# Performance work log

Hardware: AMD Instinct MI355X
Metric: run time of the kernel (lower is better)

## Reference

```python
import jax, jax.numpy as jnp
import numpy as np

D_EMB = 256
SCALE = 0.02
B, T = 4, 4096
EPS = 1e-5


def layer_norm(x, w, b):
    m = jnp.mean(x, axis=-1, keepdims=True)
    v = jnp.mean((x - m) ** 2, axis=-1, keepdims=True)
    return (x - m) * jax.lax.rsqrt(v + EPS) * w + b


def setup_inputs() -> dict:
    key = jax.random.key(0)
    ks = jax.random.split(key, 4)
    x = jax.random.normal(ks[0], (B, T, D_EMB), dtype=jnp.float32)
    qkv = jax.random.normal(ks[1], (3, D_EMB, D_EMB), dtype=jnp.float32) * SCALE
    # nn.Linear(D, 2D, bias=False): weight shape (2D, D), applied as x @ W.T
    w1 = jax.random.normal(ks[2], (2 * D_EMB, D_EMB), dtype=jnp.float32) * (1.0 / np.sqrt(D_EMB))
    w2 = jax.random.normal(ks[3], (D_EMB, 2 * D_EMB), dtype=jnp.float32) * (1.0 / np.sqrt(2 * D_EMB))
    ones = jnp.ones((D_EMB,), dtype=jnp.float32)
    zeros = jnp.zeros((D_EMB,), dtype=jnp.float32)
    return {
        "x": x, "qkv": qkv,
        "ln_q_w": ones, "ln_q_b": zeros,
        "ln_k_w": ones, "ln_k_b": zeros,
        "ln_attn_w": ones, "ln_attn_b": zeros,
        "w1": w1, "w2": w2,
        "ln_ff_w": ones, "ln_ff_b": zeros,
    }


def reference(x, qkv, ln_q_w, ln_q_b, ln_k_w, ln_k_b, ln_attn_w, ln_attn_b, w1, w2, ln_ff_w, ln_ff_b):
    # QKV projections: [3, B, T, D]
    y = jnp.einsum('btd,ndD->nbtD', x, qkv)
    q, k, v = y[0], y[1], y[2]
    q = layer_norm(q, ln_q_w, ln_q_b)
    k = layer_norm(k, ln_k_w, ln_k_b)
    # full (non-causal) single-head attention, scale by sqrt(D_EMB)
    scores = jnp.einsum('btd,bsd->bts', q, k) / jnp.sqrt(jnp.float32(D_EMB))
    attn = jax.nn.softmax(scores, axis=-1)
    y = jnp.einsum('bts,bsd->btd', attn, v)
    y = layer_norm(y, ln_attn_w, ln_attn_b)
    x = 0.7 * (x + y)
    # FFN with dual leaky_relu
    y = jax.nn.leaky_relu(x @ w1.T, negative_slope=0.2)
    y = jax.nn.leaky_relu(y @ w2.T, negative_slope=0.2)
    y = layer_norm(y, ln_ff_w, ln_ff_b)
    return 0.7 * (x + y)
```

## Files before the change

kernel.cpp:

```cpp
#include <hip/hip_runtime.h>

#define BSZ   4
#define TSEQ  4096
#define DEMB  256
#define NTOK  (BSZ * TSEQ)
#define HID   512
#define SPLITS 4
#define KEYS_PER_SPLIT (TSEQ / SPLITS)
#define TK 32
#define NT (KEYS_PER_SPLIT / TK)
#define KIMG_STRIDE 8704
#define VIMG_STRIDE 10240

using bf16x8 = __attribute__((ext_vector_type(8))) short;
using f32x16 = __attribute__((ext_vector_type(16))) float;

static __device__ __forceinline__ unsigned short f2bf(float f) {
  union { float f; unsigned u; } v; v.f = f;
  unsigned r = v.u + 0x7FFF + ((v.u >> 16) & 1);
  return (unsigned short)(r >> 16);
}
static __device__ __forceinline__ float bf2f(unsigned short u) {
  union { unsigned u; float f; } v; v.u = ((unsigned)u) << 16;
  return v.f;
}

static __device__ __forceinline__ void async16(void* lds, const void* gp) {
  __builtin_amdgcn_global_load_lds(
      (const __attribute__((address_space(1))) unsigned int*)gp,
      (__attribute__((address_space(3))) unsigned int*)lds, 16, 0, 0);
}

__global__ __launch_bounds__(256) void prep_kernel(
    const float* __restrict__ qkv, const float* __restrict__ w1,
    const float* __restrict__ w2, unsigned short* __restrict__ qkvT,
    unsigned short* __restrict__ w1b, unsigned short* __restrict__ w2b)
{
  const int tid = threadIdx.x;
  if (blockIdx.y < 3) {
    if (blockIdx.x >= 16) return;
    __shared__ float Ts[64][65];
    const int z  = blockIdx.y;
    const int k0 = (blockIdx.x >> 2) * 64;
    const int j0 = (blockIdx.x & 3) * 64;
    const float* src = qkv + (size_t)z * DEMB * DEMB + (size_t)k0 * DEMB + j0;
#pragma unroll
    for (int p = 0; p < 4; ++p) {
      int idx = p * 256 + tid;
      int r = idx >> 4, g = idx & 15;
      float4 v = *(const float4*)(src + (size_t)r * DEMB + g * 4);
      Ts[r][g * 4 + 0] = v.x; Ts[r][g * 4 + 1] = v.y;
      Ts[r][g * 4 + 2] = v.z; Ts[r][g * 4 + 3] = v.w;
    }
    __syncthreads();
    unsigned short* dst = qkvT + (size_t)z * DEMB * DEMB + (size_t)j0 * DEMB + k0;
#pragma unroll
    for (int p = 0; p < 4; ++p) {
      int idx = p * 256 + tid;
      int r = idx >> 4, g = idx & 15;
      ushort4 o;
      o.x = f2bf(Ts[g * 4 + 0][r]); o.y = f2bf(Ts[g * 4 + 1][r]);
      o.z = f2bf(Ts[g * 4 + 2][r]); o.w = f2bf(Ts[g * 4 + 3][r]);
      *(ushort4*)(dst + (size_t)r * DEMB + g * 4) = o;
    }
  } else {
    const float* s = (blockIdx.y == 3) ? w1 : w2;
    unsigned short* d = (blockIdx.y == 3) ? w1b : w2b;
    const int i = blockIdx.x * 256 + tid;
    float4 v = ((const float4*)s)[i];
    ushort4 o;
    o.x = f2bf(v.x); o.y = f2bf(v.y); o.z = f2bf(v.z); o.w = f2bf(v.w);
    ((ushort4*)d)[i] = o;
  }
}

__global__ __launch_bounds__(512, 1) void qkvln_kernel(
    const float* __restrict__ x, const unsigned short* __restrict__ qkvT,
    const float* __restrict__ lnqw, const float* __restrict__ lnqb,
    const float* __restrict__ lnkw, const float* __restrict__ lnkb,
    unsigned short* __restrict__ Qbn, unsigned short* __restrict__ Kimg,
    unsigned short* __restrict__ Vimg)
{
  __shared__ __align__(16) unsigned short sh[36864];
  unsigned short* As = sh;
  unsigned short* Bs = sh + 256 * 72;

  const int tid = threadIdx.x;
  const int w   = tid >> 6;
  const int l   = tid & 63;
  const int lm  = l & 31;
  const int lh  = l >> 5;
  const int z   = blockIdx.y;
  const int m0  = blockIdx.x * 256;
  const int bb  = m0 >> 12;

  const unsigned short* Bt = qkvT + (size_t)z * DEMB * DEMB;

  f32x16 o[8];
#pragma unroll
  for (int t = 0; t < 8; ++t)
#pragma unroll
    for (int r = 0; r < 16; ++r) o[t][r] = 0.f;

  const int fr = tid >> 4;
  const int fc = (tid & 15) * 4;

  float4 arf[8];
  bf16x8 brb[4];

#pragma unroll
  for (int i = 0; i < 8; ++i)
    arf[i] = *(const float4*)(x + (size_t)(m0 + fr + 32 * i) * DEMB + fc);
#pragma unroll
  for (int i = 0; i < 4; ++i) {
    const int c = tid + 512 * i;
    brb[i] = *(const bf16x8*)(Bt + (size_t)(c >> 3) * DEMB + (c & 7) * 8);
  }

  for (int k0 = 0; k0 < DEMB; k0 += 64) {
    __syncthreads();
#pragma unroll
    for (int i = 0; i < 8; ++i) {
      ushort4 u;
      u.x = f2bf(arf[i].x); u.y = f2bf(arf[i].y);
      u.z = f2bf(arf[i].z); u.w = f2bf(arf[i].w);
      *(ushort4*)&As[(fr + 32 * i) * 72 + fc] = u;
    }
#pragma unroll
    for (int i = 0; i < 4; ++i) {
      const int c = tid + 512 * i;
      *(bf16x8*)&Bs[(c >> 3) * 72 + (c & 7) * 8] = brb[i];
    }
    __syncthreads();

    if (k0 + 64 < DEMB) {
      const int kn = k0 + 64;
#pragma unroll
      for (int i = 0; i < 8; ++i)
        arf[i] = *(const float4*)(x + (size_t)(m0 + fr + 32 * i) * DEMB + kn + fc);
#pragma unroll
      for (int i = 0; i < 4; ++i) {
        const int c = tid + 512 * i;
        brb[i] = *(const bf16x8*)(Bt + (size_t)(c >> 3) * DEMB + kn + (c & 7) * 8);
      }
    }

#pragma unroll
    for (int ks = 0; ks < 4; ++ks) {
      bf16x8 a = *(const bf16x8*)&As[(w * 32 + lm) * 72 + ks * 16 + lh * 8];
#pragma unroll
      for (int t = 0; t < 8; ++t) {
        bf16x8 b = *(const bf16x8*)&Bs[(t * 32 + lm) * 72 + ks * 16 + lh * 8];
        o[t] = __builtin_amdgcn_mfma_f32_32x32x16_bf16(a, b, o[t], 0, 0, 0);
      }
    }
  }

  __syncthreads();

  if (z < 2) {
    const float* wp = z ? lnkw : lnqw;
    const float* bp = z ? lnkb : lnqb;
    float wc[8], bc[8];
#pragma unroll
    for (int t = 0; t < 8; ++t) { wc[t] = wp[t * 32 + lm]; bc[t] = bp[t * 32 + lm]; }
#pragma unroll
    for (int r = 0; r < 16; ++r) {
      float sv = 0.f, sq = 0.f;
#pragma unroll
      for (int t = 0; t < 8; ++t) { const float v = o[t][r]; sv += v; sq += v * v; }
#pragma unroll
      for (int d = 1; d < 32; d <<= 1) { sv += __shfl_xor(sv, d, 64); sq += __shfl_xor(sq, d, 64); }
      const float mean = sv * (1.f / DEMB);
      const float rs = rsqrtf(sq * (1.f / DEMB) - mean * mean + 1e-5f);
      const int token = m0 + w * 32 + (r & 3) + 8 * (r >> 2) + 4 * lh;
      if (z == 0) {
        unsigned short* dst = Qbn + (size_t)token * DEMB;
#pragma unroll
        for (int t = 0; t < 8; ++t)
          dst[t * 32 + lm] = f2bf((o[t][r] - mean) * rs * wc[t] + bc[t]);
      } else {
        const int t5 = token & 4095;
        unsigned short* dst =
            Kimg + (size_t)(bb * 128 + (t5 >> 5)) * KIMG_STRIDE + (t5 & 31) * 264;
#pragma unroll
        for (int t = 0; t < 8; ++t)
          dst[t * 32 + lm] = f2bf((o[t][r] - mean) * rs * wc[t] + bc[t]);
      }
    }
  } else {
#pragma unroll
    for (int h = 0; h < 2; ++h) {
      if (h) __syncthreads();
#pragma unroll
      for (int t2 = 0; t2 < 4; ++t2) {
        const int t = h * 4 + t2;
#pragma unroll
        for (int r = 0; r < 16; ++r) {
          const int row = w * 32 + (r & 3) + 8 * (r >> 2) + 4 * lh;
          sh[row * 130 + t2 * 32 + lm] = f2bf(o[t][r]);
        }
      }
      __syncthreads();
      const int d2 = tid & 127;
      const int tq = tid >> 7;
      const int d  = h * 128 + d2;
#pragma unroll
      for (int j = 0; j < 16; ++j) {
        const int tok0 = tq * 64 + j * 4;
        ushort4 v;
        v.x = sh[(tok0 + 0) * 130 + d2];
        v.y = sh[(tok0 + 1) * 130 + d2];
        v.z = sh[(tok0 + 2) * 130 + d2];
        v.w = sh[(tok0 + 3) * 130 + d2];
        const int gtok = m0 + tok0;
        const int kt = (gtok & 4095) >> 5;
        *(ushort4*)(Vimg + (size_t)(bb * 128 + kt) * VIMG_STRIDE + d * 40 + (tok0 & 31)) = v;
      }
    }
  }
}

__global__ __launch_bounds__(256, 3) void gemm_ffn_kernel(
    const unsigned short* __restrict__ A, const unsigned short* __restrict__ Bt,
    unsigned short* __restrict__ C, int M, int N, int K)
{
  __shared__ __align__(16) unsigned short As[128 * 72];
  __shared__ __align__(16) unsigned short Bs[128 * 72];

  const int tid = threadIdx.x;
  const int w   = tid >> 6;
  const int wm  = w >> 1, wn = w & 1;
  const int l   = tid & 63;
  const int lm  = l & 31;
  const int lh  = l >> 5;

  const int m0    = blockIdx.x * 128;
  const int nbase = blockIdx.y * 128;

  f32x16 acc00, acc01, acc10, acc11;
#pragma unroll
  for (int r = 0; r < 16; ++r) { acc00[r] = 0.f; acc01[r] = 0.f; acc10[r] = 0.f; acc11[r] = 0.f; }

  const int lr = tid >> 3;
  const int lc = (tid & 7) * 8;

  bf16x8 arb[4], brb[4];

#pragma unroll
  for (int i = 0; i < 4; ++i) {
    arb[i] = *(const bf16x8*)(A  + (size_t)(m0 + i * 32 + lr) * K + lc);
    brb[i] = *(const bf16x8*)(Bt + (size_t)(nbase + i * 32 + lr) * K + lc);
  }

  for (int k0 = 0; k0 < K; k0 += 64) {
    __syncthreads();
#pragma unroll
    for (int i = 0; i < 4; ++i) {
      *(bf16x8*)&As[(i * 32 + lr) * 72 + lc] = arb[i];
      *(bf16x8*)&Bs[(i * 32 + lr) * 72 + lc] = brb[i];
    }
    __syncthreads();

    if (k0 + 64 < K) {
      const int kn = k0 + 64;
#pragma unroll
      for (int i = 0; i < 4; ++i) {
        arb[i] = *(const bf16x8*)(A  + (size_t)(m0 + i * 32 + lr) * K + kn + lc);
        brb[i] = *(const bf16x8*)(Bt + (size_t)(nbase + i * 32 + lr) * K + kn + lc);
      }
    }

#pragma unroll
    for (int ks = 0; ks < 4; ++ks) {
      bf16x8 a0 = *(const bf16x8*)&As[(wm * 64 + lm)      * 72 + ks * 16 + lh * 8];
      bf16x8 a1 = *(const bf16x8*)&As[(wm * 64 + 32 + lm) * 72 + ks * 16 + lh * 8];
      bf16x8 b0 = *(const bf16x8*)&Bs[(wn * 64 + lm)      * 72 + ks * 16 + lh * 8];
      bf16x8 b1 = *(const bf16x8*)&Bs[(wn * 64 + 32 + lm) * 72 + ks * 16 + lh * 8];
      acc00 = __builtin_amdgcn_mfma_f32_32x32x16_bf16(a0, b0, acc00, 0, 0, 0);
      acc01 = __builtin_amdgcn_mfma_f32_32x32x16_bf16(a0, b1, acc01, 0, 0, 0);
      acc10 = __builtin_amdgcn_mfma_f32_32x32x16_bf16(a1, b0, acc10, 0, 0, 0);
      acc11 = __builtin_amdgcn_mfma_f32_32x32x16_bf16(a1, b1, acc11, 0, 0, 0);
    }
  }

  const f32x16* accs[4] = { &acc00, &acc01, &acc10, &acc11 };
#pragma unroll
  for (int am = 0; am < 2; ++am)
#pragma unroll
    for (int bn = 0; bn < 2; ++bn) {
      const f32x16& a = *accs[am * 2 + bn];
#pragma unroll
      for (int r = 0; r < 16; ++r) {
        const int m = m0 + wm * 64 + am * 32 + (r & 3) + 8 * (r >> 2) + 4 * lh;
        const int n = nbase + wn * 64 + bn * 32 + lm;
        float v = a[r];
        v = v > 0.f ? v : 0.2f * v;
        C[(size_t)m * N + n] = f2bf(v);
      }
    }
}

__global__ __launch_bounds__(256) void ln_res_bf16_kernel(
    const unsigned short* __restrict__ Y, const float* __restrict__ Xin,
    const float* __restrict__ w, const float* __restrict__ b,
    float* __restrict__ Out)
{
  const int lane = threadIdx.x & 63;
  const size_t row = (size_t)blockIdx.x * 4 + (threadIdx.x >> 6);
  ushort4 u = *(const ushort4*)&Y[row * DEMB + lane * 4];
  float y0 = bf2f(u.x), y1 = bf2f(u.y), y2 = bf2f(u.z), y3 = bf2f(u.w);
  float s  = y0 + y1 + y2 + y3;
  float sq = y0 * y0 + y1 * y1 + y2 * y2 + y3 * y3;
#pragma unroll
  for (int o = 32; o > 0; o >>= 1) { s += __shfl_down(s, o); sq += __shfl_down(sq, o); }
  s = __shfl(s, 0); sq = __shfl(sq, 0);
  const float m  = s * (1.f / DEMB);
  const float rs = rsqrtf(sq * (1.f / DEMB) - m * m + 1e-5f);
  const float4 wv = *(const float4*)&w[lane * 4];
  const float4 bv = *(const float4*)&b[lane * 4];
  const float4 xi = *(const float4*)&Xin[row * DEMB + lane * 4];
  float4 o;
  o.x = 0.7f * (xi.x + (y0 - m) * rs * wv.x + bv.x);
  o.y = 0.7f * (xi.y + (y1 - m) * rs * wv.y + bv.y);
  o.z = 0.7f * (xi.z + (y2 - m) * rs * wv.z + bv.z);
  o.w = 0.7f * (xi.w + (y3 - m) * rs * wv.w + bv.w);
  *(float4*)&Out[row * DEMB + lane * 4] = o;
}

__global__ __launch_bounds__(512) void attn_split_kernel(
    const unsigned short* __restrict__ Qb, const unsigned short* __restrict__ Kimg,
    const unsigned short* __restrict__ Vimg, unsigned short* __restrict__ Opart,
    float* __restrict__ lpart)
{
  __shared__ __align__(16) unsigned short Ks[2][KIMG_STRIDE];
  __shared__ __align__(16) unsigned short Vs[3][VIMG_STRIDE];
  __shared__ __align__(16) unsigned short Pb[8 * 32 * 40];

  const int tid = threadIdx.x;
  const int w   = tid >> 6;
  const int l   = tid & 63;
  const int lm  = l & 31;
  const int lh  = l >> 5;

  const int lin = blockIdx.x;
  const int xcd = lin & 7;
  const int idx = lin >> 3;
  const int b     = xcd >> 1;
  const int split = (xcd & 1) * 2 + (idx & 1);
  const int q0    = (idx >> 1) * 256;

  const unsigned short* Qbase  = Qb + (size_t)b * TSEQ * DEMB;
  const unsigned short* Ktiles = Kimg + (size_t)(b * 128 + split * 32) * KIMG_STRIDE;
  const unsigned short* Vtiles = Vimg + (size_t)(b * 128 + split * 32) * VIMG_STRIDE;

  bf16x8 qf[16];
  {
    const unsigned short* qrow = Qbase + (size_t)(q0 + w * 32 + lm) * DEMB + lh * 8;
#pragma unroll
    for (int ks = 0; ks < 16; ++ks) qf[ks] = *(const bf16x8*)(qrow + ks * 16);
  }

  f32x16 o[8];
  float lsum[16], spv[16];
#pragma unroll
  for (int t = 0; t < 8; ++t)
#pragma unroll
    for (int r = 0; r < 16; ++r) o[t][r] = 0.f;
#pragma unroll
  for (int r = 0; r < 16; ++r) lsum[r] = 0.f;

  unsigned short* Pw = &Pb[w * 32 * 40];

#pragma unroll
  for (int i = 0; i < 3; ++i) {
    const int c = w + 8 * i;
    if (c < 17) async16(&Ks[0][c * 512], Ktiles + c * 512 + l * 8);
  }
#pragma unroll
  for (int i = 0; i < 3; ++i) {
    const int c = w + 8 * i;
    if (c < 20) async16(&Vs[0][c * 512], Vtiles + c * 512 + l * 8);
  }

  {
    __syncthreads();
#pragma unroll
    for (int i = 0; i < 3; ++i) {
      const int c = w + 8 * i;
      if (c < 17) async16(&Ks[1][c * 512], Ktiles + (size_t)KIMG_STRIDE + c * 512 + l * 8);
    }
#pragma unroll
    for (int i = 0; i < 3; ++i) {
      const int c = w + 8 * i;
      if (c < 20) async16(&Vs[1][c * 512], Vtiles + (size_t)VIMG_STRIDE + c * 512 + l * 8);
    }
    f32x16 s;
#pragma unroll
    for (int r = 0; r < 16; ++r) s[r] = 0.f;
#pragma unroll
    for (int ks = 0; ks < 16; ++ks) {
      bf16x8 kf = *(const bf16x8*)&Ks[0][lm * 264 + ks * 16 + lh * 8];
      s = __builtin_amdgcn_mfma_f32_32x32x16_bf16(qf[ks], kf, s, 0, 0, 0);
    }
#pragma unroll
    for (int r = 0; r < 16; ++r) spv[r] = s[r];
  }

  int vprev = 0, vcur = 1, vnext = 2;

  for (int st = 1; st < NT; ++st) {
    __syncthreads();

    if (st + 1 < NT) {
      const unsigned short* kn = Ktiles + (size_t)(st + 1) * KIMG_STRIDE;
      const unsigned short* vn = Vtiles + (size_t)(st + 1) * VIMG_STRIDE;
#pragma unroll
      for (int i = 0; i < 3; ++i) {
        const int c = w + 8 * i;
        if (c < 17) async16(&Ks[(st + 1) & 1][c * 512], kn + c * 512 + l * 8);
      }
#pragma unroll
      for (int i = 0; i < 3; ++i) {
        const int c = w + 8 * i;
        if (c < 20) async16(&Vs[vnext][c * 512], vn + c * 512 + l * 8);
      }
    }

#pragma unroll
    for (int r = 0; r < 16; ++r) {
      const float pv = exp2f(spv[r] * 0.09016844335f - 11.541560327f);
      lsum[r] += pv;
      const int row = (r & 3) + ((r >> 2) << 3) + (lh << 2);
      Pw[row * 40 + lm] = f2bf(pv);
    }
    {
      const unsigned short* Vp = &Vs[vprev][0];
#pragma unroll
      for (int ks = 0; ks < 2; ++ks) {
        bf16x8 pf = *(const bf16x8*)&Pw[lm * 40 + ks * 16 + lh * 8];
#pragma unroll
        for (int t = 0; t < 8; ++t) {
          bf16x8 vf = *(const bf16x8*)&Vp[(t * 32 + lm) * 40 + ks * 16 + lh * 8];
          o[t] = __builtin_amdgcn_mfma_f32_32x32x16_bf16(pf, vf, o[t], 0, 0, 0);
        }
      }
    }

    {
      f32x16 s;
#pragma unroll
      for (int r = 0; r < 16; ++r) s[r] = 0.f;
      const unsigned short* Kp = &Ks[st & 1][0];
#pragma unroll
      for (int ks = 0; ks < 16; ++ks) {
        bf16x8 kf = *(const bf16x8*)&Kp[lm * 264 + ks * 16 + lh * 8];
        s = __builtin_amdgcn_mfma_f32_32x32x16_bf16(qf[ks], kf, s, 0, 0, 0);
      }
#pragma unroll
      for (int r = 0; r < 16; ++r) spv[r] = s[r];
    }

    const int tmp = vprev; vprev = vcur; vcur = vnext; vnext = tmp;
  }

#pragma unroll
  for (int r = 0; r < 16; ++r) {
    const float pv = exp2f(spv[r] * 0.09016844335f - 11.541560327f);
    lsum[r] += pv;
    const int row = (r & 3) + ((r >> 2) << 3) + (lh << 2);
    Pw[row * 40 + lm] = f2bf(pv);
  }
  {
    const unsigned short* Vp = &Vs[vprev][0];
#pragma unroll
    for (int ks = 0; ks < 2; ++ks) {
      bf16x8 pf = *(const bf16x8*)&Pw[lm * 40 + ks * 16 + lh * 8];
#pragma unroll
      for (int t = 0; t < 8; ++t) {
        bf16x8 vf = *(const bf16x8*)&Vp[(t * 32 + lm) * 40 + ks * 16 + lh * 8];
        o[t] = __builtin_amdgcn_mfma_f32_32x32x16_bf16(pf, vf, o[t], 0, 0, 0);
      }
    }
  }

#pragma unroll
  for (int r = 0; r < 16; ++r) {
#pragma unroll
    for (int d = 1; d < 32; d <<= 1) lsum[r] += __shfl_xor(lsum[r], d, 64);
  }
  unsigned short* Ob =
      Opart + ((size_t)split * NTOK + (size_t)b * TSEQ + q0 + w * 32) * DEMB;
  float* lb = lpart + (size_t)split * NTOK + (size_t)b * TSEQ + q0 + w * 32;
#pragma unroll
  for (int r = 0; r < 16; ++r) {
    const int row = (r & 3) + ((r >> 2) << 3) + (lh << 2);
#pragma unroll
    for (int t = 0; t < 8; ++t)
      Ob[(size_t)row * DEMB + t * 32 + lm] = f2bf(o[t][r]);
    if (lm == 0) lb[row] = lsum[r];
  }
}

__global__ __launch_bounds__(256) void combine_lnres_kernel(
    const unsigned short* __restrict__ Opart, const float* __restrict__ lpart,
    const float* __restrict__ Xin, const float* __restrict__ w,
    const float* __restrict__ b, float* __restrict__ Out,
    unsigned short* __restrict__ Outb)
{
  const int lane = threadIdx.x & 63;
  const size_t row = (size_t)blockIdx.x * 4 + (threadIdx.x >> 6);
  float4 acc = make_float4(0.f, 0.f, 0.f, 0.f);
  float lt = 0.f;
#pragma unroll
  for (int p = 0; p < SPLITS; ++p) {
    const ushort4 u = *(const ushort4*)&Opart[((size_t)p * NTOK + row) * DEMB + lane * 4];
    acc.x += bf2f(u.x); acc.y += bf2f(u.y);
    acc.z += bf2f(u.z); acc.w += bf2f(u.w);
    lt += lpart[(size_t)p * NTOK + row];
  }
  const float inv = 1.f / lt;
  const float y0 = acc.x * inv, y1 = acc.y * inv, y2 = acc.z * inv, y3 = acc.w * inv;
  float s  = y0 + y1 + y2 + y3;
  float sq = y0 * y0 + y1 * y1 + y2 * y2 + y3 * y3;
#pragma unroll
  for (int o = 32; o > 0; o >>= 1) { s += __shfl_down(s, o); sq += __shfl_down(sq, o); }
  s = __shfl(s, 0); sq = __shfl(sq, 0);
  const float m  = s * (1.f / DEMB);
  const float rs = rsqrtf(sq * (1.f / DEMB) - m * m + 1e-5f);
  const float4 wv = *(const float4*)&w[lane * 4];
  const float4 bv = *(const float4*)&b[lane * 4];
  const float4 xi = *(const float4*)&Xin[row * DEMB + lane * 4];
  float4 o;
  o.x = 0.7f * (xi.x + (y0 - m) * rs * wv.x + bv.x);
  o.y = 0.7f * (xi.y + (y1 - m) * rs * wv.y + bv.y);
  o.z = 0.7f * (xi.z + (y2 - m) * rs * wv.z + bv.z);
  o.w = 0.7f * (xi.w + (y3 - m) * rs * wv.w + bv.w);
  *(float4*)&Out[row * DEMB + lane * 4] = o;
  ushort4 ob;
  ob.x = f2bf(o.x); ob.y = f2bf(o.y); ob.z = f2bf(o.z); ob.w = f2bf(o.w);
  *(ushort4*)&Outb[row * DEMB + lane * 4] = ob;
}

extern "C" void kernel_launch(void* const* d_in, const int* in_sizes, int n_in,
                              void* d_out, int out_size, void* d_ws, size_t ws_size,
                              hipStream_t stream)
{
  (void)in_sizes; (void)n_in; (void)out_size; (void)ws_size;
  const float* x    = (const float*)d_in[0];
  const float* qkv  = (const float*)d_in[1];
  const float* lnqw = (const float*)d_in[2];
  const float* lnqb = (const float*)d_in[3];
  const float* lnkw = (const float*)d_in[4];
  const float* lnkb = (const float*)d_in[5];
  const float* lnaw = (const float*)d_in[6];
  const float* lnab = (const float*)d_in[7];
  const float* w1   = (const float*)d_in[8];
  const float* w2   = (const float*)d_in[9];
  const float* lnfw = (const float*)d_in[10];
  const float* lnfb = (const float*)d_in[11];
  float* out = (float*)d_out;

  char* W = (char*)d_ws;
  const size_t MB = 1 << 20;
  unsigned short* Qbn   = (unsigned short*)(W + 0);
  unsigned short* Kimg  = (unsigned short*)(W + 8 * MB);
  unsigned short* Vimg  = (unsigned short*)(W + 17 * MB);
  unsigned short* Opart = (unsigned short*)(W + 28 * MB);
  float*          lpart = (float*)(W + 60 * MB);
  unsigned short* x1b   = (unsigned short*)(W + 0);
  unsigned short* H     = (unsigned short*)(W + 8 * MB);
  unsigned short* Y2b   = (unsigned short*)(W + 28 * MB);
  unsigned short* qkvT  = (unsigned short*)(W + 60 * MB + 512 * 1024);
  unsigned short* w1b   = (unsigned short*)(W + 61 * MB);
  unsigned short* w2b   = (unsigned short*)(W + 61 * MB + 256 * 1024);

  const dim3 blk(256);

  prep_kernel<<<dim3(128, 5), blk, 0, stream>>>(qkv, w1, w2, qkvT, w1b, w2b);

  qkvln_kernel<<<dim3(NTOK / 256, 3), dim3(512), 0, stream>>>(
      x, qkvT, lnqw, lnqb, lnkw, lnkb, Qbn, Kimg, Vimg);

  attn_split_kernel<<<dim3(256), dim3(512), 0, stream>>>(Qbn, Kimg, Vimg, Opart, lpart);
  combine_lnres_kernel<<<NTOK / 4, blk, 0, stream>>>(Opart, lpart, x, lnaw, lnab, out, x1b);

  gemm_ffn_kernel<<<dim3(NTOK / 128, HID / 128), blk, 0, stream>>>(
      x1b, w1b, H, NTOK, HID, DEMB);
  gemm_ffn_kernel<<<dim3(NTOK / 128, DEMB / 128), blk, 0, stream>>>(
      H, w2b, Y2b, NTOK, DEMB, HID);

  ln_res_bf16_kernel<<<NTOK / 4, blk, 0, stream>>>(Y2b, out, lnfw, lnfb, out);
}
```

Baseline: 226.8 us.

## Restructure attention split kernel: register-resident P via permlane swap, smaller blocks

Rewrites the attention split kernel to compute S transposed (K as the A operand) so the exponentiated probabilities can be packed to bf16 with v_cvt_pk_bf16_f32 and rearranged with permlane32_swap directly into the PV MFMA operand layout. This removes the shared-memory round trip for P and the cross-lane row-sum reduction, replacing them with one lane-pair shuffle. Blocks shrink to 256 threads over 128 queries with 512 blocks and two blocks per CU. The software pipeline drops from triple-buffered V with lookahead QK to plain double buffering, and s_setprio is added around the MFMA sections. The simpler pipeline gives up the QK/softmax overlap in exchange for fewer LDS ops and higher occupancy.

```diff
diff --git a/kernel.cpp b/kernel.cpp
--- a/kernel.cpp
+++ b/kernel.cpp
@@ -29,6 +29,12 @@
   __builtin_amdgcn_global_load_lds(
       (const __attribute__((address_space(1))) unsigned int*)gp,
       (__attribute__((address_space(3))) unsigned int*)lds, 16, 0, 0);
+}
+
+static __device__ __forceinline__ void plswap(unsigned& a, unsigned& b) {
+  using uint2v = __attribute__((ext_vector_type(2))) unsigned int;
+  uint2v r = __builtin_amdgcn_permlane32_swap(a, b, false, false);
+  a = r[0]; b = r[1];
 }
 
 __global__ __launch_bounds__(256) void prep_kernel(
@@ -328,14 +334,13 @@
   *(float4*)&Out[row * DEMB + lane * 4] = o;
 }
 
-__global__ __launch_bounds__(512) void attn_split_kernel(
+__global__ __launch_bounds__(256, 2) void attn_split_kernel(
     const unsigned short* __restrict__ Qb, const unsigned short* __restrict__ Kimg,
     const unsigned short* __restrict__ Vimg, unsigned short* __restrict__ Opart,
     float* __restrict__ lpart)
 {
   __shared__ __align__(16) unsigned short Ks[2][KIMG_STRIDE];
-  __shared__ __align__(16) unsigned short Vs[3][VIMG_STRIDE];
-  __shared__ __align__(16) unsigned short Pb[8 * 32 * 40];
+  __shared__ __align__(16) unsigned short Vs[2][VIMG_STRIDE];
 
   const int tid = threadIdx.x;
   const int w   = tid >> 6;
@@ -348,7 +353,7 @@
   const int idx = lin >> 3;
   const int b     = xcd >> 1;
   const int split = (xcd & 1) * 2 + (idx & 1);
-  const int q0    = (idx >> 1) * 256;
+  const int q0    = (idx >> 1) * 128;
 
   const unsigned short* Qbase  = Qb + (size_t)b * TSEQ * DEMB;
   const unsigned short* Ktiles = Kimg + (size_t)(b * 128 + split * 32) * KIMG_STRIDE;
@@ -362,133 +367,87 @@
   }
 
   f32x16 o[8];
-  float lsum[16], spv[16];
 #pragma unroll
   for (int t = 0; t < 8; ++t)
 #pragma unroll
     for (int r = 0; r < 16; ++r) o[t][r] = 0.f;
-#pragma unroll
-  for (int r = 0; r < 16; ++r) lsum[r] = 0.f;
-
-  unsigned short* Pw = &Pb[w * 32 * 40];
-
-#pragma unroll
-  for (int i = 0; i < 3; ++i) {
-    const int c = w + 8 * i;
+  float psum = 0.f;
+
+#pragma unroll
+  for (int i = 0; i < 5; ++i) {
+    const int c = w + 4 * i;
     if (c < 17) async16(&Ks[0][c * 512], Ktiles + c * 512 + l * 8);
   }
 #pragma unroll
-  for (int i = 0; i < 3; ++i) {
-    const int c = w + 8 * i;
-    if (c < 20) async16(&Vs[0][c * 512], Vtiles + c * 512 + l * 8);
-  }
-
-  {
-    __syncthreads();
-#pragma unroll
-    for (int i = 0; i < 3; ++i) {
-      const int c = w + 8 * i;
-      if (c < 17) async16(&Ks[1][c * 512], Ktiles + (size_t)KIMG_STRIDE + c * 512 + l * 8);
-    }
-#pragma unroll
-    for (int i = 0; i < 3; ++i) {
-      const int c = w + 8 * i;
-      if (c < 20) async16(&Vs[1][c * 512], Vtiles + (size_t)VIMG_STRIDE + c * 512 + l * 8);
-    }
-    f32x16 s;
-#pragma unroll
-    for (int r = 0; r < 16; ++r) s[r] = 0.f;
-#pragma unroll
-    for (int ks = 0; ks < 16; ++ks) {
-      bf16x8 kf = *(const bf16x8*)&Ks[0][lm * 264 + ks * 16 + lh * 8];
-      s = __builtin_amdgcn_mfma_f32_32x32x16_bf16(qf[ks], kf, s, 0, 0, 0);
-    }
-#pragma unroll
-    for (int r = 0; r < 16; ++r) spv[r] = s[r];
-  }
-
-  int vprev = 0, vcur = 1, vnext = 2;
-
-  for (int st = 1; st < NT; ++st) {
-    __syncthreads();
+  for (int i = 0; i < 5; ++i) {
+    const int c = w + 4 * i;
+    async16(&Vs[0][c * 512], Vtiles + c * 512 + l * 8);
+  }
+  __syncthreads();
+
+  for (int st = 0; st < NT; ++st) {
+    const int cur = st & 1;
 
     if (st + 1 < NT) {
       const unsigned short* kn = Ktiles + (size_t)(st + 1) * KIMG_STRIDE;
       const unsigned short* vn = Vtiles + (size_t)(st + 1) * VIMG_STRIDE;
-#pragma unroll
-      for (int i = 0; i < 3; ++i) {
-        const int c = w + 8 * i;
-        if (c < 17) async16(&Ks[(st + 1) & 1][c * 512], kn + c * 512 + l * 8);
-      }
-#pragma unroll
-      for (int i = 0; i < 3; ++i) {
-        const int c = w + 8 * i;
-        if (c < 20) async16(&Vs[vnext][c * 512], vn + c * 512 + l * 8);
-      }
-    }
-
-#pragma unroll
-    for (int r = 0; r < 16; ++r) {
-      const float pv = exp2f(spv[r] * 0.09016844335f - 11.541560327f);
-      lsum[r] += pv;
-      const int row = (r & 3) + ((r >> 2) << 3) + (lh << 2);
-      Pw[row * 40 + lm] = f2bf(pv);
-    }
-    {
-      const unsigned short* Vp = &Vs[vprev][0];
-#pragma unroll
-      for (int ks = 0; ks < 2; ++ks) {
-        bf16x8 pf = *(const bf16x8*)&Pw[lm * 40 + ks * 16 + lh * 8];
-#pragma unroll
-        for (int t = 0; t < 8; ++t) {
-          bf16x8 vf = *(const bf16x8*)&Vp[(t * 32 + lm) * 40 + ks * 16 + lh * 8];
-          o[t] = __builtin_amdgcn_mfma_f32_32x32x16_bf16(pf, vf, o[t], 0, 0, 0);
-        }
-      }
-    }
-
-    {
-      f32x16 s;
-#pragma unroll
-      for (int r = 0; r < 16; ++r) s[r] = 0.f;
-      const unsigned short* Kp = &Ks[st & 1][0];
-#pragma unroll
-      for (int ks = 0; ks < 16; ++ks) {
-        bf16x8 kf = *(const bf16x8*)&Kp[lm * 264 + ks * 16 + lh * 8];
-        s = __builtin_amdgcn_mfma_f32_32x32x16_bf16(qf[ks], kf, s, 0, 0, 0);
-      }
-#pragma unroll
-      for (int r = 0; r < 16; ++r) spv[r] = s[r];
-    }
-
-    const int tmp = vprev; vprev = vcur; vcur = vnext; vnext = tmp;
-  }
-
-#pragma unroll
-  for (int r = 0; r < 16; ++r) {
-    const float pv = exp2f(spv[r] * 0.09016844335f - 11.541560327f);
-    lsum[r] += pv;
-    const int row = (r & 3) + ((r >> 2) << 3) + (lh << 2);
-    Pw[row * 40 + lm] = f2bf(pv);
-  }
-  {
-    const unsigned short* Vp = &Vs[vprev][0];
-#pragma unroll
-    for (int ks = 0; ks < 2; ++ks) {
-      bf16x8 pf = *(const bf16x8*)&Pw[lm * 40 + ks * 16 + lh * 8];
-#pragma unroll
-      for (int t = 0; t < 8; ++t) {
-        bf16x8 vf = *(const bf16x8*)&Vp[(t * 32 + lm) * 40 + ks * 16 + lh * 8];
-        o[t] = __builtin_amdgcn_mfma_f32_32x32x16_bf16(pf, vf, o[t], 0, 0, 0);
-      }
-    }
-  }
-
-#pragma unroll
-  for (int r = 0; r < 16; ++r) {
-#pragma unroll
-    for (int d = 1; d < 32; d <<= 1) lsum[r] += __shfl_xor(lsum[r], d, 64);
-  }
+      const int nxt = cur ^ 1;
+#pragma unroll
+      for (int i = 0; i < 5; ++i) {
+        const int c = w + 4 * i;
+        if (c < 17) async16(&Ks[nxt][c * 512], kn + c * 512 + l * 8);
+      }
+#pragma unroll
+      for (int i = 0; i < 5; ++i) {
+        const int c = w + 4 * i;
+        async16(&Vs[nxt][c * 512], vn + c * 512 + l * 8);
+      }
+    }
+
+    f32x16 s;
+#pragma unroll
+    for (int r = 0; r < 16; ++r) s[r] = 0.f;
+    const unsigned short* Kp = &Ks[cur][0];
+    __builtin_amdgcn_s_setprio(1);
+#pragma unroll
+    for (int ks = 0; ks < 16; ++ks) {
+      bf16x8 kf = *(const bf16x8*)&Kp[lm * 264 + ks * 16 + lh * 8];
+      s = __builtin_amdgcn_mfma_f32_32x32x16_bf16(kf, qf[ks], s, 0, 0, 0);
+    }
+    __builtin_amdgcn_s_setprio(0);
+
+    unsigned pk[8];
+#pragma unroll
+    for (int i = 0; i < 8; ++i) {
+      const float e0 = exp2f(s[2 * i]     * 0.09016844335f - 11.541560327f);
+      const float e1 = exp2f(s[2 * i + 1] * 0.09016844335f - 11.541560327f);
+      psum += e0 + e1;
+      asm("v_cvt_pk_bf16_f32 %0, %1, %2" : "=v"(pk[i]) : "v"(e0), "v"(e1));
+    }
+    plswap(pk[0], pk[2]);
+    plswap(pk[1], pk[3]);
+    plswap(pk[4], pk[6]);
+    plswap(pk[5], pk[7]);
+    union U8 { unsigned u[4]; bf16x8 v; } pfa, pfb;
+    pfa.u[0] = pk[0]; pfa.u[1] = pk[1]; pfa.u[2] = pk[2]; pfa.u[3] = pk[3];
+    pfb.u[0] = pk[4]; pfb.u[1] = pk[5]; pfb.u[2] = pk[6]; pfb.u[3] = pk[7];
+
+    const unsigned short* Vp = &Vs[cur][0];
+    __builtin_amdgcn_s_setprio(1);
+#pragma unroll
+    for (int t = 0; t < 8; ++t) {
+      bf16x8 vf0 = *(const bf16x8*)&Vp[(t * 32 + lm) * 40 + lh * 8];
+      o[t] = __builtin_amdgcn_mfma_f32_32x32x16_bf16(pfa.v, vf0, o[t], 0, 0, 0);
+      bf16x8 vf1 = *(const bf16x8*)&Vp[(t * 32 + lm) * 40 + 16 + lh * 8];
+      o[t] = __builtin_amdgcn_mfma_f32_32x32x16_bf16(pfb.v, vf1, o[t], 0, 0, 0);
+    }
+    __builtin_amdgcn_s_setprio(0);
+
+    __syncthreads();
+  }
+
+  const float tot = psum + __shfl_xor(psum, 32, 64);
+
   unsigned short* Ob =
       Opart + ((size_t)split * NTOK + (size_t)b * TSEQ + q0 + w * 32) * DEMB;
   float* lb = lpart + (size_t)split * NTOK + (size_t)b * TSEQ + q0 + w * 32;
@@ -498,8 +457,8 @@
 #pragma unroll
     for (int t = 0; t < 8; ++t)
       Ob[(size_t)row * DEMB + t * 32 + lm] = f2bf(o[t][r]);
-    if (lm == 0) lb[row] = lsum[r];
-  }
+  }
+  if (lh == 0) lb[lm] = tot;
 }
 
 __global__ __launch_bounds__(256) void combine_lnres_kernel(
@@ -582,7 +541,7 @@
   qkvln_kernel<<<dim3(NTOK / 256, 3), dim3(512), 0, stream>>>(
       x, qkvT, lnqw, lnqb, lnkw, lnkb, Qbn, Kimg, Vimg);
 
-  attn_split_kernel<<<dim3(256), dim3(512), 0, stream>>>(Qbn, Kimg, Vimg, Opart, lpart);
+  attn_split_kernel<<<dim3(512), dim3(256), 0, stream>>>(Qbn, Kimg, Vimg, Opart, lpart);
   combine_lnres_kernel<<<NTOK / 4, blk, 0, stream>>>(Opart, lpart, x, lnaw, lnab, out, x1b);
 
   gemm_ffn_kernel<<<dim3(NTOK / 128, HID / 128), blk, 0, stream>>>(
```

After: 226.9 us. About the same (+0.0%).
